# Kernel tuning notes

Measured on AMD Instinct MI355X. Metric: run time of the kernel, lower is better.

The kernel has to match this reference:

```python
import jax, jax.numpy as jnp
import numpy as np

N1, N2, P, D = 8, 8, 1024, 768  # 8 query / 8 normal images, 32x32 patches, ViT-B dim
PH = PW = 32
H = W = 512


def setup_inputs() -> dict:
    key = jax.random.key(0)
    k1, k2 = jax.random.split(key)
    feats = jax.random.normal(k1, (N1, P, D), dtype=jnp.float32)
    nfeats = jax.random.normal(k2, (N2, P, D), dtype=jnp.float32)
    return {"feats": feats, "nfeats": nfeats, "ph": PH, "pw": PW, "h": H, "w": W}


def _bilinear_resize(x, out_h, out_w):
    # x: [N, h, w] -> [N, out_h, out_w]; matches F.interpolate(mode='bilinear', align_corners=False)
    n, h, w = x.shape
    sy = (jnp.arange(out_h, dtype=x.dtype) + 0.5) * (h / out_h) - 0.5
    sx = (jnp.arange(out_w, dtype=x.dtype) + 0.5) * (w / out_w) - 0.5
    y0f = jnp.floor(sy)
    x0f = jnp.floor(sx)
    wy = (sy - y0f)[None, :, None]  # [1, out_h, 1]
    wx = (sx - x0f)[None, None, :]  # [1, 1, out_w]
    y0 = jnp.clip(y0f.astype(jnp.int32), 0, h - 1)
    y1 = jnp.clip(y0f.astype(jnp.int32) + 1, 0, h - 1)
    x0 = jnp.clip(x0f.astype(jnp.int32), 0, w - 1)
    x1 = jnp.clip(x0f.astype(jnp.int32) + 1, 0, w - 1)
    v00 = x[:, y0[:, None], x0[None, :]]
    v01 = x[:, y0[:, None], x1[None, :]]
    v10 = x[:, y1[:, None], x0[None, :]]
    v11 = x[:, y1[:, None], x1[None, :]]
    top = v00 * (1 - wx) + v01 * wx
    bot = v10 * (1 - wx) + v11 * wx
    return top * (1 - wy) + bot * wy


def reference(feats, nfeats, ph, pw, h, w):
    # L2-normalize patch embeddings (as in forward: f / f.norm(dim=-1, keepdim=True))
    f = feats / jnp.linalg.norm(feats, axis=-1, keepdims=True)   # [N1, P, D]
    g = nfeats / jnp.linalg.norm(nfeats, axis=-1, keepdims=True)  # [N2, P, D]
    n1 = f.shape[0]
    # cdist(feats.reshape(N1*P,D), nfeats.reshape(N2*P,D)).reshape(N1,P,N2,P).permute(0,2,1,3)
    gram = jnp.einsum('npd,mqd->nmpq', f, g)                      # [N1, N2, P, P]
    fa2 = jnp.sum(f * f, axis=-1)                                 # [N1, P]
    gb2 = jnp.sum(g * g, axis=-1)                                 # [N2, P]
    d2 = fa2[:, None, :, None] + gb2[None, :, None, :] - 2.0 * gram
    dist = jnp.sqrt(jnp.maximum(d2, 0.0)) * 0.5                   # distances / 2
    # nearest-normal-patch distance per query patch (bg mask is all ones here)
    scores_patch = jnp.min(dist, axis=-1)                         # [N1, N2, P]
    scores = jnp.mean(jnp.max(scores_patch, axis=-1), axis=1)     # [N1]
    sp = jnp.mean(scores_patch, axis=1).reshape(n1, ph, pw)       # [N1, PH, PW]
    scores_pixel = _bilinear_resize(sp, h, w)                     # [N1, H, W]
    return scores, scores_pixel
```

## Files before the change

### kernel.cpp

```cpp
#include <hip/hip_runtime.h>
#include <hip/hip_bf16.h>
#include <stdint.h>

#define N1 8
#define N2 8
#define PP 1024
#define DD 768
#define PH 32
#define PW 32
#define OH 512
#define OW 512

#define NKT 12

typedef int i32x4 __attribute__((ext_vector_type(4)));

__global__ __launch_bounds__(256) void nrm_kernel(
    const float* __restrict__ inA, const float* __restrict__ inB,
    char* __restrict__ outA, char* __restrict__ outB) {
  int row = blockIdx.x;
  const float* src;
  char* dst;
  if (row < N1 * PP) {
    src = inA + (size_t)row * DD;
    dst = outA + (size_t)row * DD;
  } else {
    row -= N1 * PP;
    src = inB + (size_t)row * DD;
    dst = outB + (size_t)row * DD;
  }
  const int t = threadIdx.x;
  const float v0 = src[t], v1 = src[t + 256], v2 = src[t + 512];
  float s = v0 * v0 + v1 * v1 + v2 * v2;
#pragma unroll
  for (int m = 32; m; m >>= 1) s += __shfl_xor(s, m, 64);
  __shared__ float red[4];
  const int wave = t >> 6, lane = t & 63;
  if (lane == 0) red[wave] = s;
  __syncthreads();
  const float inv = 127.0f / sqrtf(red[0] + red[1] + red[2] + red[3]);
  dst[t]       = (char)__float2int_rn(v0 * inv);
  dst[t + 256] = (char)__float2int_rn(v1 * inv);
  dst[t + 512] = (char)__float2int_rn(v2 * inv);
}

__device__ __forceinline__ void gll16(const char* src, char* dst) {
  __builtin_amdgcn_global_load_lds(
      (const __attribute__((address_space(1))) void*)src,
      (__attribute__((address_space(3))) void*)dst, 16, 0, 0);
}

__global__ __launch_bounds__(512, 2) void grami8_kernel(
    const char* __restrict__ fq, const char* __restrict__ gq,
    int* __restrict__ rowmaxI) {
  __shared__ __align__(16) char lds[8][8192];

  const int bid = blockIdx.x;
  const int wg = (bid & 7) * 128 + (bid >> 3);
  const int pair = wg >> 4;
  const int tile = wg & 15;
  const int fn = pair >> 3, gm = pair & 7;
  const int mt = tile >> 2, nt = tile & 3;
  const int brow = mt * 256, bcol = nt * 256;

  const int t = threadIdx.x;
  const int lane = t & 63, wave = t >> 6;
  const int lr = lane & 15, lk = lane >> 4;
  const int wr = wave >> 2, wc = wave & 3;

  const char* rowA = fq + ((size_t)fn * PP + brow) * DD;
  const char* rowB = gq + ((size_t)gm * PP + bcol) * DD;

  const int xs = (t * 16) ^ (((t >> 3) & 7) << 4);
  const int srow = xs >> 6;
  const int scol = xs & 63;

  const int swzv = ((lr >> 1) & 7) << 4;
  const int abase = (lr * 64 + lk * 16) ^ swzv;
  const int bbase = (wc & 1) * 4096 + ((lr * 64 + lk * 16) ^ swzv);

#define AHALF(d) (&lds[(d) * 4 + wr][0])
#define BHALF(d) (&lds[(d) * 4 + 2 + (wc >> 1)][0])
#define STAGE(rowPtr, h, kt, hbase)                                       \
  gll16(rowPtr + (size_t)((h) * 128 + srow) * DD + (kt) * 64 + scol,      \
        (hbase) + t * 16)

  i32x4 acc[8][4];
#pragma unroll
  for (int i = 0; i < 8; ++i)
#pragma unroll
    for (int j = 0; j < 4; ++j) acc[i][j] = (i32x4){0, 0, 0, 0};

  STAGE(rowB, 0, 0, &lds[0 * 4 + 2 + 0][0]);
  STAGE(rowB, 1, 0, &lds[0 * 4 + 2 + 1][0]);
  STAGE(rowA, 0, 0, &lds[0 * 4 + 0][0]);
  STAGE(rowA, 1, 0, &lds[0 * 4 + 1][0]);
  STAGE(rowB, 0, 1, &lds[1 * 4 + 2 + 0][0]);
  STAGE(rowB, 1, 1, &lds[1 * 4 + 2 + 1][0]);
  STAGE(rowA, 0, 1, &lds[1 * 4 + 0][0]);
  STAGE(rowA, 1, 1, &lds[1 * 4 + 1][0]);
  asm volatile("s_waitcnt vmcnt(4)" ::: "memory");
  __builtin_amdgcn_s_barrier();

  i32x4 a[4], b01[2], b23[2];

#pragma unroll 1
  for (int k = 0; k < NKT; ++k) {
    const int d = k & 1;
    const char* Ab = AHALF(d);
    const char* Bb = BHALF(d);
    const bool st = (k + 2 < NKT);

    a[0] = *(const i32x4*)(Ab + abase + 0 * 1024);
    a[1] = *(const i32x4*)(Ab + abase + 1 * 1024);
    a[2] = *(const i32x4*)(Ab + abase + 2 * 1024);
    a[3] = *(const i32x4*)(Ab + abase + 3 * 1024);
    b01[0] = *(const i32x4*)(Bb + bbase + 0 * 1024);
    b01[1] = *(const i32x4*)(Bb + bbase + 1 * 1024);
    __builtin_amdgcn_s_barrier();
    asm volatile("s_waitcnt lgkmcnt(0)" ::: "memory");
    __builtin_amdgcn_sched_barrier(0);
    __builtin_amdgcn_s_setprio(1);
#pragma unroll
    for (int m = 0; m < 4; ++m)
#pragma unroll
      for (int n = 0; n < 2; ++n)
        acc[m][n] = __builtin_amdgcn_mfma_i32_16x16x64_i8(a[m], b01[n],
                                                          acc[m][n], 0, 0, 0);
    __builtin_amdgcn_s_setprio(0);
    __builtin_amdgcn_sched_barrier(0);
    __builtin_amdgcn_s_barrier();

    b23[0] = *(const i32x4*)(Bb + bbase + 2 * 1024);
    b23[1] = *(const i32x4*)(Bb + bbase + 3 * 1024);
    __builtin_amdgcn_s_barrier();
    asm volatile("s_waitcnt lgkmcnt(0)" ::: "memory");
    __builtin_amdgcn_sched_barrier(0);
    __builtin_amdgcn_s_setprio(1);
#pragma unroll
    for (int m = 0; m < 4; ++m)
#pragma unroll
      for (int n = 0; n < 2; ++n)
        acc[m][n + 2] = __builtin_amdgcn_mfma_i32_16x16x64_i8(
            a[m], b23[n], acc[m][n + 2], 0, 0, 0);
    __builtin_amdgcn_s_setprio(0);
    __builtin_amdgcn_sched_barrier(0);
    __builtin_amdgcn_s_barrier();

    a[0] = *(const i32x4*)(Ab + abase + 4 * 1024);
    a[1] = *(const i32x4*)(Ab + abase + 5 * 1024);
    a[2] = *(const i32x4*)(Ab + abase + 6 * 1024);
    a[3] = *(const i32x4*)(Ab + abase + 7 * 1024);
    if (st) {
      STAGE(rowB, 0, k + 2, &lds[d * 4 + 2 + 0][0]);
      STAGE(rowB, 1, k + 2, &lds[d * 4 + 2 + 1][0]);
    }
    __builtin_amdgcn_s_barrier();
    asm volatile("s_waitcnt lgkmcnt(0)" ::: "memory");
    __builtin_amdgcn_sched_barrier(0);
    __builtin_amdgcn_s_setprio(1);
#pragma unroll
    for (int m = 0; m < 4; ++m)
#pragma unroll
      for (int n = 0; n < 2; ++n)
        acc[m + 4][n + 2] = __builtin_amdgcn_mfma_i32_16x16x64_i8(
            a[m], b23[n], acc[m + 4][n + 2], 0, 0, 0);
    __builtin_amdgcn_s_setprio(0);
    __builtin_amdgcn_sched_barrier(0);
    __builtin_amdgcn_s_barrier();

    if (st) {
      STAGE(rowA, 0, k + 2, &lds[d * 4 + 0][0]);
      STAGE(rowA, 1, k + 2, &lds[d * 4 + 1][0]);
    }
    __builtin_amdgcn_s_barrier();
    __builtin_amdgcn_s_setprio(1);
#pragma unroll
    for (int m = 0; m < 4; ++m)
#pragma unroll
      for (int n = 0; n < 2; ++n)
        acc[m + 4][n] = __builtin_amdgcn_mfma_i32_16x16x64_i8(
            a[m], b01[n], acc[m + 4][n], 0, 0, 0);
    __builtin_amdgcn_s_setprio(0);
    __builtin_amdgcn_sched_barrier(0);
    if (k <= NKT - 3) {
      asm volatile("s_waitcnt vmcnt(4)" ::: "memory");
    } else if (k == NKT - 2) {
      asm volatile("s_waitcnt vmcnt(0)" ::: "memory");
    }
    if (k < NKT - 1) __builtin_amdgcn_s_barrier();
  }

  int* rm = rowmaxI + (size_t)(fn * 8 + gm) * PP;
#pragma unroll
  for (int m = 0; m < 8; ++m) {
#pragma unroll
    for (int r = 0; r < 4; ++r) {
      int vv = max(max(acc[m][0][r], acc[m][1][r]),
                   max(acc[m][2][r], acc[m][3][r]));
      vv = max(vv, __shfl_xor(vv, 1, 64));
      vv = max(vv, __shfl_xor(vv, 2, 64));
      vv = max(vv, __shfl_xor(vv, 4, 64));
      vv = max(vv, __shfl_xor(vv, 8, 64));
      if (lr == 0) {
        const int row = brow + wr * 128 + m * 16 + lk * 4 + r;
        atomicMax(&rm[row], vv);
      }
    }
  }
#undef AHALF
#undef BHALF
#undef STAGE
}

__global__ __launch_bounds__(256) void finalize_kernel(
    const int* __restrict__ rowmaxI, float* __restrict__ sp,
    float* __restrict__ scores) {
  const int n = blockIdx.x, t = threadIdx.x;
  const int lane = t & 63, wave = t >> 6;
  __shared__ float red[4];
  __shared__ float maxd[N2];
  float spacc[4] = {0.f, 0.f, 0.f, 0.f};
  for (int m = 0; m < N2; ++m) {
    float lmax = -1e30f;
#pragma unroll
    for (int i = 0; i < 4; ++i) {
      const int p = t + i * 256;
      const float g = (float)rowmaxI[(size_t)(n * N2 + m) * PP + p] *
                      (1.0f / 16129.0f);
      const float d = 0.5f * sqrtf(fmaxf(0.f, 2.f - 2.f * g));
      spacc[i] += d;
      lmax = fmaxf(lmax, d);
    }
#pragma unroll
    for (int msk = 32; msk; msk >>= 1) lmax = fmaxf(lmax, __shfl_xor(lmax, msk, 64));
    if (lane == 0) red[wave] = lmax;
    __syncthreads();
    if (t == 0) maxd[m] = fmaxf(fmaxf(red[0], red[1]), fmaxf(red[2], red[3]));
    __syncthreads();
  }
  if (t == 0) {
    float s = 0.f;
    for (int m = 0; m < N2; ++m) s += maxd[m];
    scores[n] = s * (1.0f / N2);
  }
#pragma unroll
  for (int i = 0; i < 4; ++i)
    sp[(size_t)n * PP + t + i * 256] = spacc[i] * (1.0f / N2);
}

__global__ __launch_bounds__(256) void resize_kernel(
    const float* __restrict__ sp, float* __restrict__ out) {
  const int idx = blockIdx.x * 256 + threadIdx.x;
  const int ox = idx & (OW - 1);
  const int oy = (idx >> 9) & (OH - 1);
  const int n = idx >> 18;
  const float sy = (oy + 0.5f) * ((float)PH / OH) - 0.5f;
  const float sx = (ox + 0.5f) * ((float)PW / OW) - 0.5f;
  const float y0f = floorf(sy), x0f = floorf(sx);
  const float wy = sy - y0f, wx = sx - x0f;
  int y0 = (int)y0f, x0 = (int)x0f;
  int y1 = y0 + 1, x1 = x0 + 1;
  y0 = min(max(y0, 0), PH - 1);
  y1 = min(max(y1, 0), PH - 1);
  x0 = min(max(x0, 0), PW - 1);
  x1 = min(max(x1, 0), PW - 1);
  const float* s = sp + (size_t)n * PP;
  const float v00 = s[y0 * PW + x0], v01 = s[y0 * PW + x1];
  const float v10 = s[y1 * PW + x0], v11 = s[y1 * PW + x1];
  const float top = v00 * (1.f - wx) + v01 * wx;
  const float bot = v10 * (1.f - wx) + v11 * wx;
  out[idx] = top * (1.f - wy) + bot * wy;
}

extern "C" void kernel_launch(void* const* d_in, const int* in_sizes, int n_in,
                              void* d_out, int out_size, void* d_ws, size_t ws_size,
                              hipStream_t stream) {
  const float* feats = (const float*)d_in[0];
  const float* nfeats = (const float*)d_in[1];
  float* out = (float*)d_out;

  char* ws = (char*)d_ws;
  const size_t FQ_BYTES = (size_t)N1 * PP * DD;
  char* fq = ws;
  char* gq = ws + FQ_BYTES;
  int* rowmaxI = (int*)(ws + 2 * FQ_BYTES);
  float* sp = (float*)(ws + 2 * FQ_BYTES + (size_t)N1 * N2 * PP * 4);

  hipMemsetAsync(rowmaxI, 0x80, (size_t)N1 * N2 * PP * 4, stream);

  nrm_kernel<<<(N1 + N2) * PP, 256, 0, stream>>>(feats, nfeats, fq, gq);

  grami8_kernel<<<1024, 512, 0, stream>>>(fq, gq, rowmaxI);

  finalize_kernel<<<N1, 256, 0, stream>>>(rowmaxI, sp, out);
  resize_kernel<<<(N1 * OH * OW) / 256, 256, 0, stream>>>(sp, out + 8);
}
```

Baseline: 121.6 us.

## Replace ping-pong LDS schedule with 4-slot ring buffer and prefetch depth three

The int8 GEMM main loop moves from a double-buffered LDS layout to a 4-slot ring. Three k-tiles are prefetched ahead, and the four interleaved compute phases, each with its own barriers, collapse into one load-all-fragments then 32-MFMA block with a single barrier per iteration. The aim is to cut barrier and synchronisation overhead and hide global-load latency better. In exchange, LDS per block doubles to 128 KB, so two blocks no longer fit per CU, which may lower occupancy and latency hiding. It also raises register pressure from holding all A and B fragments at once.

Measured after the change: 121.2 us. Within noise of the previous version (-0.4%).

```diff
diff --git a/kernel.cpp b/kernel.cpp
--- a/kernel.cpp
+++ b/kernel.cpp
@@ -53,7 +53,7 @@
 __global__ __launch_bounds__(512, 2) void grami8_kernel(
     const char* __restrict__ fq, const char* __restrict__ gq,
     int* __restrict__ rowmaxI) {
-  __shared__ __align__(16) char lds[8][8192];
+  __shared__ __align__(16) char lds[4][4][8192];
 
   const int bid = blockIdx.x;
   const int wg = (bid & 7) * 128 + (bid >> 3);
@@ -79,11 +79,9 @@
   const int abase = (lr * 64 + lk * 16) ^ swzv;
   const int bbase = (wc & 1) * 4096 + ((lr * 64 + lk * 16) ^ swzv);
 
-#define AHALF(d) (&lds[(d) * 4 + wr][0])
-#define BHALF(d) (&lds[(d) * 4 + 2 + (wc >> 1)][0])
-#define STAGE(rowPtr, h, kt, hbase)                                       \
+#define STAGE(rowPtr, h, kt, slotptr)                                     \
   gll16(rowPtr + (size_t)((h) * 128 + srow) * DD + (kt) * 64 + scol,      \
-        (hbase) + t * 16)
+        (slotptr) + t * 16)
 
   i32x4 acc[8][4];
 #pragma unroll
@@ -91,104 +89,54 @@
 #pragma unroll
     for (int j = 0; j < 4; ++j) acc[i][j] = (i32x4){0, 0, 0, 0};
 
-  STAGE(rowB, 0, 0, &lds[0 * 4 + 2 + 0][0]);
-  STAGE(rowB, 1, 0, &lds[0 * 4 + 2 + 1][0]);
-  STAGE(rowA, 0, 0, &lds[0 * 4 + 0][0]);
-  STAGE(rowA, 1, 0, &lds[0 * 4 + 1][0]);
-  STAGE(rowB, 0, 1, &lds[1 * 4 + 2 + 0][0]);
-  STAGE(rowB, 1, 1, &lds[1 * 4 + 2 + 1][0]);
-  STAGE(rowA, 0, 1, &lds[1 * 4 + 0][0]);
-  STAGE(rowA, 1, 1, &lds[1 * 4 + 1][0]);
-  asm volatile("s_waitcnt vmcnt(4)" ::: "memory");
+#pragma unroll
+  for (int kk = 0; kk < 3; ++kk) {
+    STAGE(rowB, 0, kk, &lds[kk][2][0]);
+    STAGE(rowB, 1, kk, &lds[kk][3][0]);
+    STAGE(rowA, 0, kk, &lds[kk][0][0]);
+    STAGE(rowA, 1, kk, &lds[kk][1][0]);
+  }
+  asm volatile("s_waitcnt vmcnt(8)" ::: "memory");
   __builtin_amdgcn_s_barrier();
-
-  i32x4 a[4], b01[2], b23[2];
+  asm volatile("" ::: "memory");
 
 #pragma unroll 1
   for (int k = 0; k < NKT; ++k) {
-    const int d = k & 1;
-    const char* Ab = AHALF(d);
-    const char* Bb = BHALF(d);
-    const bool st = (k + 2 < NKT);
-
-    a[0] = *(const i32x4*)(Ab + abase + 0 * 1024);
-    a[1] = *(const i32x4*)(Ab + abase + 1 * 1024);
-    a[2] = *(const i32x4*)(Ab + abase + 2 * 1024);
-    a[3] = *(const i32x4*)(Ab + abase + 3 * 1024);
-    b01[0] = *(const i32x4*)(Bb + bbase + 0 * 1024);
-    b01[1] = *(const i32x4*)(Bb + bbase + 1 * 1024);
-    __builtin_amdgcn_s_barrier();
-    asm volatile("s_waitcnt lgkmcnt(0)" ::: "memory");
-    __builtin_amdgcn_sched_barrier(0);
-    __builtin_amdgcn_s_setprio(1);
-#pragma unroll
-    for (int m = 0; m < 4; ++m)
-#pragma unroll
-      for (int n = 0; n < 2; ++n)
-        acc[m][n] = __builtin_amdgcn_mfma_i32_16x16x64_i8(a[m], b01[n],
+    const char* Ab = &lds[k & 3][wr][0];
+    const char* Bb = &lds[k & 3][2 + (wc >> 1)][0];
+
+    i32x4 a[8], b[4];
+#pragma unroll
+    for (int m = 0; m < 8; ++m)
+      a[m] = *(const i32x4*)(Ab + abase + m * 1024);
+#pragma unroll
+    for (int n = 0; n < 4; ++n)
+      b[n] = *(const i32x4*)(Bb + bbase + n * 1024);
+
+    if (k + 3 < NKT) {
+      const int ss = (k + 3) & 3;
+      STAGE(rowB, 0, k + 3, &lds[ss][2][0]);
+      STAGE(rowB, 1, k + 3, &lds[ss][3][0]);
+      STAGE(rowA, 0, k + 3, &lds[ss][0][0]);
+      STAGE(rowA, 1, k + 3, &lds[ss][1][0]);
+    }
+
+#pragma unroll
+    for (int m = 0; m < 8; ++m)
+#pragma unroll
+      for (int n = 0; n < 4; ++n)
+        acc[m][n] = __builtin_amdgcn_mfma_i32_16x16x64_i8(a[m], b[n],
                                                           acc[m][n], 0, 0, 0);
-    __builtin_amdgcn_s_setprio(0);
-    __builtin_amdgcn_sched_barrier(0);
-    __builtin_amdgcn_s_barrier();
-
-    b23[0] = *(const i32x4*)(Bb + bbase + 2 * 1024);
-    b23[1] = *(const i32x4*)(Bb + bbase + 3 * 1024);
-    __builtin_amdgcn_s_barrier();
-    asm volatile("s_waitcnt lgkmcnt(0)" ::: "memory");
-    __builtin_amdgcn_sched_barrier(0);
-    __builtin_amdgcn_s_setprio(1);
-#pragma unroll
-    for (int m = 0; m < 4; ++m)
-#pragma unroll
-      for (int n = 0; n < 2; ++n)
-        acc[m][n + 2] = __builtin_amdgcn_mfma_i32_16x16x64_i8(
-            a[m], b23[n], acc[m][n + 2], 0, 0, 0);
-    __builtin_amdgcn_s_setprio(0);
-    __builtin_amdgcn_sched_barrier(0);
-    __builtin_amdgcn_s_barrier();
-
-    a[0] = *(const i32x4*)(Ab + abase + 4 * 1024);
-    a[1] = *(const i32x4*)(Ab + abase + 5 * 1024);
-    a[2] = *(const i32x4*)(Ab + abase + 6 * 1024);
-    a[3] = *(const i32x4*)(Ab + abase + 7 * 1024);
-    if (st) {
-      STAGE(rowB, 0, k + 2, &lds[d * 4 + 2 + 0][0]);
-      STAGE(rowB, 1, k + 2, &lds[d * 4 + 2 + 1][0]);
-    }
-    __builtin_amdgcn_s_barrier();
-    asm volatile("s_waitcnt lgkmcnt(0)" ::: "memory");
-    __builtin_amdgcn_sched_barrier(0);
-    __builtin_amdgcn_s_setprio(1);
-#pragma unroll
-    for (int m = 0; m < 4; ++m)
-#pragma unroll
-      for (int n = 0; n < 2; ++n)
-        acc[m + 4][n + 2] = __builtin_amdgcn_mfma_i32_16x16x64_i8(
-            a[m], b23[n], acc[m + 4][n + 2], 0, 0, 0);
-    __builtin_amdgcn_s_setprio(0);
-    __builtin_amdgcn_sched_barrier(0);
-    __builtin_amdgcn_s_barrier();
-
-    if (st) {
-      STAGE(rowA, 0, k + 2, &lds[d * 4 + 0][0]);
-      STAGE(rowA, 1, k + 2, &lds[d * 4 + 1][0]);
-    }
-    __builtin_amdgcn_s_barrier();
-    __builtin_amdgcn_s_setprio(1);
-#pragma unroll
-    for (int m = 0; m < 4; ++m)
-#pragma unroll
-      for (int n = 0; n < 2; ++n)
-        acc[m + 4][n] = __builtin_amdgcn_mfma_i32_16x16x64_i8(
-            a[m], b01[n], acc[m + 4][n], 0, 0, 0);
-    __builtin_amdgcn_s_setprio(0);
-    __builtin_amdgcn_sched_barrier(0);
-    if (k <= NKT - 3) {
+
+    if (k < NKT - 3) {
+      asm volatile("s_waitcnt vmcnt(8)" ::: "memory");
+    } else if (k == NKT - 3) {
       asm volatile("s_waitcnt vmcnt(4)" ::: "memory");
     } else if (k == NKT - 2) {
       asm volatile("s_waitcnt vmcnt(0)" ::: "memory");
     }
-    if (k < NKT - 1) __builtin_amdgcn_s_barrier();
+    __builtin_amdgcn_s_barrier();
+    asm volatile("" ::: "memory");
   }
 
   int* rm = rowmaxI + (size_t)(fn * 8 + gm) * PP;
@@ -208,8 +156,6 @@
       }
     }
   }
-#undef AHALF
-#undef BHALF
 #undef STAGE
 }
 
```
